# Performance work log

Measured on AMD Instinct MI355X. Metric: run time of the kernel, lower is better.

## Reference

```python
import jax, jax.numpy as jnp
import numpy as np

N = 4096      # sequence length (tokens)
D = 256       # model_dim
H = 4         # num_heads
DH = D // H   # dim_per_head = 64
TOPK = 30     # dot_attention default
SCALE = float((DH // H) ** -0.5)  # torch: (key.size(-1)//num_heads)**-0.5 = 16**-0.5 = 0.25
LN_EPS = 1e-5


def setup_inputs() -> dict:
    key = jax.random.key(0)
    ks = jax.random.split(key, 11)
    s = 0.02
    return {
        "key_in":   jax.random.normal(ks[0], (N, D), jnp.float32),
        "value_in": jax.random.normal(ks[1], (N, D), jnp.float32),
        "query_in": jax.random.normal(ks[2], (N, D), jnp.float32),
        "Wq": jax.random.normal(ks[3], (D, D), jnp.float32) * s,
        "bq": jax.random.normal(ks[4], (D,), jnp.float32) * s,
        "Wk": jax.random.normal(ks[5], (D, D), jnp.float32) * s,
        "bk": jax.random.normal(ks[6], (D,), jnp.float32) * s,
        "Wv": jax.random.normal(ks[7], (D, D), jnp.float32) * s,
        "bv": jax.random.normal(ks[8], (D,), jnp.float32) * s,
        "Wo": jax.random.normal(ks[9], (D, D), jnp.float32) * s,
        "bo": jax.random.normal(ks[10], (D,), jnp.float32) * s,
        "ln_g": jnp.ones((D,), jnp.float32),
        "ln_b": jnp.zeros((D,), jnp.float32),
    }


def reference(key_in, value_in, query_in, Wq, bq, Wk, bk, Wv, bv, Wo, bo, ln_g, ln_b):
    # Projections (nn.Linear: x @ W.T + b)
    q = query_in @ Wq.T + bq            # (N, D)
    k = key_in @ Wk.T + bk
    v = value_in @ Wv.T + bv
    # view(N, H, DH).transpose(0,1) -> (H, N, DH)
    qh = q.reshape(N, H, DH).transpose(1, 0, 2)
    kh = k.reshape(N, H, DH).transpose(1, 0, 2)
    vh = v.reshape(N, H, DH).transpose(1, 0, 2)

    scores = jnp.einsum('hnd,hmd->hnm', qh, kh) * SCALE   # (H, N, N)

    # top-k mask via scatter (faithful to torch.topk + scatter_)
    idx = jax.lax.top_k(scores, TOPK)[1]                  # (H, N, TOPK)
    mask = jnp.zeros_like(scores).at[
        jnp.arange(H)[:, None, None],
        jnp.arange(N)[None, :, None],
        idx].set(1.0)
    masked = jnp.where(mask > 0, scores, -jnp.inf)
    attn = jax.nn.softmax(masked, axis=-1)                # (H, N, N); dropout p=0 -> identity

    ctx = jnp.einsum('hnm,hmd->hnd', attn, vh)            # (H, N, DH)
    ctx = ctx.transpose(1, 0, 2).reshape(N, D)

    out = ctx @ Wo.T + bo
    resid = query_in + out                                # residual is pre-projection query
    mu = resid.mean(axis=-1, keepdims=True)
    var = resid.var(axis=-1, keepdims=True)               # biased var, like torch LayerNorm
    out = (resid - mu) / jnp.sqrt(var + LN_EPS) * ln_g + ln_b
    return out, attn
```

## Files before the change

### kernel.cpp

```cpp
#include <hip/hip_runtime.h>
#include <stdint.h>

#define N_TOK 4096
#define DIM   256
#define NH    4
#define DH    64
#define TOPK  30
#define CANDN 40
#define HWIN  128u
#define ATT_SCALE 0.25f
#define LN_EPS 1e-5f

typedef __attribute__((ext_vector_type(8))) short bf16x8;
typedef __attribute__((ext_vector_type(4))) float f32x4;

static __device__ __forceinline__ ushort f2bf(float f) {
    uint x = __float_as_uint(f);
    return (ushort)((x + 0x7FFFu + ((x >> 16) & 1u)) >> 16);
}
static __device__ __forceinline__ bf16x8 load_frag(const ushort* p) {
    union { int4 i; bf16x8 f; } u;
    u.i = *reinterpret_cast<const int4*>(p);
    return u.f;
}
static __device__ __forceinline__ bf16x8 cvt_frag(const float* p) {
    float4 a = *reinterpret_cast<const float4*>(p);
    float4 b = *reinterpret_cast<const float4*>(p + 4);
    union { ushort u[8]; bf16x8 f; } u;
    u.u[0] = f2bf(a.x); u.u[1] = f2bf(a.y); u.u[2] = f2bf(a.z); u.u[3] = f2bf(a.w);
    u.u[4] = f2bf(b.x); u.u[5] = f2bf(b.y); u.u[6] = f2bf(b.z); u.u[7] = f2bf(b.w);
    return u.f;
}
static __device__ __forceinline__ uint s16key(uint u) {
    return (u & 0x8000u) ? (u ^ 0xFFFFu) : (u | 0x8000u);
}
static __device__ __forceinline__ int jdecode(int P) {
    return (P & ~127) | ((P & 7) << 4) | ((P >> 3) & 15);
}

#define BK 32
__global__ __launch_bounds__(256) void front_kernel(
    const float* __restrict__ query_in, const float* __restrict__ key_in,
    const float* __restrict__ value_in,
    const float* __restrict__ Wq, const float* __restrict__ bq,
    const float* __restrict__ Wk, const float* __restrict__ bk,
    const float* __restrict__ Wv, const float* __restrict__ bv,
    float* __restrict__ qf, float* __restrict__ kf,
    ushort* __restrict__ qb, ushort* __restrict__ kb,
    float* __restrict__ vf)
{
    if (blockIdx.x < 8) {
        const int j0g = blockIdx.x * 64;
        const int sel = j0g >> 8;
        const int j0  = j0g & 255;
        const float* A    = sel ? key_in : query_in;
        const float* W    = sel ? Wk : Wq;
        const float* bias = sel ? bk : bq;
        float*  outF = sel ? kf : qf;
        ushort* outB = sel ? kb : qb;

        __shared__ float As[BK][64 + 4];
        __shared__ float Ws[BK][64 + 4];
        const int tid = threadIdx.x;
        const int tx = tid & 15;
        const int ty = tid >> 4;
        const int i0 = blockIdx.y * 64;

        float acc[4][4];
#pragma unroll
        for (int r = 0; r < 4; r++)
#pragma unroll
            for (int c = 0; c < 4; c++) acc[r][c] = 0.f;

        for (int k0 = 0; k0 < DIM; k0 += BK) {
#pragma unroll
            for (int u = 0; u < 2; u++) {
                const int f = u * 256 + tid;
                const int r = f >> 3;
                const int c = (f & 7) * 4;
                float4 va = *reinterpret_cast<const float4*>(A + (size_t)(i0 + r) * DIM + k0 + c);
                As[c + 0][r] = va.x; As[c + 1][r] = va.y;
                As[c + 2][r] = va.z; As[c + 3][r] = va.w;
                float4 vw = *reinterpret_cast<const float4*>(W + (size_t)(j0 + r) * DIM + k0 + c);
                Ws[c + 0][r] = vw.x; Ws[c + 1][r] = vw.y;
                Ws[c + 2][r] = vw.z; Ws[c + 3][r] = vw.w;
            }
            __syncthreads();
#pragma unroll
            for (int kk = 0; kk < BK; kk++) {
                const float4 a4 = *reinterpret_cast<const float4*>(&As[kk][ty * 4]);
                const float4 b4 = *reinterpret_cast<const float4*>(&Ws[kk][tx * 4]);
                const float ar[4] = {a4.x, a4.y, a4.z, a4.w};
                const float br[4] = {b4.x, b4.y, b4.z, b4.w};
#pragma unroll
                for (int r = 0; r < 4; r++)
#pragma unroll
                    for (int c = 0; c < 4; c++) acc[r][c] += ar[r] * br[c];
            }
            __syncthreads();
        }

#pragma unroll
        for (int r = 0; r < 4; r++) {
            const int gi = i0 + ty * 4 + r;
#pragma unroll
            for (int c = 0; c < 4; c++) {
                const int gj = j0 + tx * 4 + c;
                float v = acc[r][c] + bias[gj];
                outF[(size_t)gi * DIM + gj] = v;
                outB[(size_t)gi * DIM + gj] = f2bf(v);
            }
        }
    } else {
        const int lane = threadIdx.x & 63;
        const int wv   = threadIdx.x >> 6;
        const int i0   = blockIdx.y * 64 + wv * 16;
        const int j0   = (blockIdx.x - 8) * 64;
        const int r = lane & 15, q = lane >> 4;

        f32x4 acc[4];
#pragma unroll
        for (int b = 0; b < 4; b++) acc[b] = (f32x4){0.f, 0.f, 0.f, 0.f};

#pragma unroll
        for (int ks = 0; ks < 8; ks++) {
            const int kk = ks * 32 + q * 8;
            bf16x8 af = cvt_frag(value_in + (size_t)(i0 + r) * DIM + kk);
            bf16x8 bfr[4];
#pragma unroll
            for (int jt = 0; jt < 4; jt++)
                bfr[jt] = cvt_frag(Wv + (size_t)(j0 + jt * 16 + r) * DIM + kk);
#pragma unroll
            for (int jt = 0; jt < 4; jt++)
                acc[jt] = __builtin_amdgcn_mfma_f32_16x16x32_bf16(af, bfr[jt], acc[jt], 0, 0, 0);
        }

#pragma unroll
        for (int jt = 0; jt < 4; jt++) {
            const int gj = j0 + jt * 16 + r;
            const float bvv = bv[gj];
#pragma unroll
            for (int rg = 0; rg < 4; rg++) {
                const int gi = i0 + q * 4 + rg;
                vf[(size_t)gi * DIM + gj] = acc[jt][rg] + bvv;
            }
        }
    }
}

__global__ __launch_bounds__(256) void oproj_kernel(
    const ushort* __restrict__ A, const float* __restrict__ Wo,
    const float* __restrict__ bias, const float* __restrict__ addX,
    float* __restrict__ outF)
{
    const int lane = threadIdx.x & 63;
    const int wv   = threadIdx.x >> 6;
    const int i0   = blockIdx.y * 64 + wv * 16;
    const int j0   = blockIdx.x * 64;
    const int r = lane & 15, q = lane >> 4;

    f32x4 acc[4];
#pragma unroll
    for (int b = 0; b < 4; b++) acc[b] = (f32x4){0.f, 0.f, 0.f, 0.f};

#pragma unroll
    for (int ks = 0; ks < 8; ks++) {
        const int kk = ks * 32 + q * 8;
        bf16x8 af = load_frag(A + (size_t)(i0 + r) * DIM + kk);
        bf16x8 bfr[4];
#pragma unroll
        for (int jt = 0; jt < 4; jt++)
            bfr[jt] = cvt_frag(Wo + (size_t)(j0 + jt * 16 + r) * DIM + kk);
#pragma unroll
        for (int jt = 0; jt < 4; jt++)
            acc[jt] = __builtin_amdgcn_mfma_f32_16x16x32_bf16(af, bfr[jt], acc[jt], 0, 0, 0);
    }

#pragma unroll
    for (int jt = 0; jt < 4; jt++) {
        const int gj = j0 + jt * 16 + r;
        const float bvv = bias[gj];
#pragma unroll
        for (int rg = 0; rg < 4; rg++) {
            const int gi = i0 + q * 4 + rg;
            float v = acc[jt][rg] + bvv + addX[(size_t)gi * DIM + gj];
            outF[(size_t)gi * DIM + gj] = v;
        }
    }
}

__global__ __launch_bounds__(256) void scores_kernel(
    const ushort* __restrict__ qb, const ushort* __restrict__ kb,
    ushort* __restrict__ sb)
{
    const int lane = threadIdx.x & 63;
    const int wv   = threadIdx.x >> 6;
    const int h    = blockIdx.z;
    const int i0   = blockIdx.y * 128 + wv * 32;
    const int j0   = blockIdx.x * 128;
    const int r = lane & 15, q = lane >> 4;
    const int koff = h * DH;

    f32x4 acc[2][8];
#pragma unroll
    for (int a = 0; a < 2; a++)
#pragma unroll
        for (int b = 0; b < 8; b++) acc[a][b] = (f32x4){0.f, 0.f, 0.f, 0.f};

#pragma unroll
    for (int ks = 0; ks < 2; ks++) {
        const int kk = koff + ks * 32 + q * 8;
        bf16x8 af[2], bfr[8];
#pragma unroll
        for (int mt = 0; mt < 2; mt++)
            af[mt] = load_frag(qb + (size_t)(i0 + mt * 16 + r) * DIM + kk);
#pragma unroll
        for (int jt = 0; jt < 8; jt++)
            bfr[jt] = load_frag(kb + (size_t)(j0 + jt * 16 + r) * DIM + kk);
#pragma unroll
        for (int mt = 0; mt < 2; mt++)
#pragma unroll
            for (int jt = 0; jt < 8; jt++)
                acc[mt][jt] = __builtin_amdgcn_mfma_f32_16x16x32_bf16(
                    af[mt], bfr[jt], acc[mt][jt], 0, 0, 0);
    }

    const int tileBase = (j0 >> 7) * 16;
#pragma unroll
    for (int mt = 0; mt < 2; mt++)
#pragma unroll
        for (int rg = 0; rg < 4; rg++) {
            const int gi = i0 + mt * 16 + q * 4 + rg;
            uint w4[4];
#pragma unroll
            for (int p = 0; p < 4; p++) {
                const uint klo = s16key(f2bf(acc[mt][2 * p + 0][rg]));
                const uint khi = s16key(f2bf(acc[mt][2 * p + 1][rg]));
                w4[p] = klo | (khi << 16);
            }
            int4 outv;
            outv.x = (int)w4[0]; outv.y = (int)w4[1];
            outv.z = (int)w4[2]; outv.w = (int)w4[3];
            int4* rowp = reinterpret_cast<int4*>(sb + ((size_t)(h * N_TOK + gi)) * N_TOK);
            rowp[tileBase + r] = outv;
        }
}

__global__ __launch_bounds__(256) void select_kernel(
    const ushort* __restrict__ sb, const float* __restrict__ qf,
    const float* __restrict__ kf, const float* __restrict__ vf,
    float* __restrict__ pval, int* __restrict__ pidx,
    ushort* __restrict__ ctxb)
{
    const int lane = threadIdx.x & 63;
    const int wv   = threadIdx.x >> 6;
    const int row  = blockIdx.x * 4 + wv;
    const int h    = row >> 12;
    const int i    = row & (N_TOK - 1);
    const ushort* srow = sb + (size_t)row * N_TOK;

    __shared__ uint  hist[4][256];
    __shared__ uint  cand[4][64];
    __shared__ uint  ccnt[4];
    __shared__ float pw[4][TOPK];
    __shared__ int   jw[4][TOPK];
    __shared__ __align__(16) float qsh[4][DH];

    qsh[wv][lane] = qf[(size_t)i * DIM + h * DH + lane];
    if (lane == 0) ccnt[wv] = 0;
#pragma unroll
    for (int b = 0; b < 4; b++) hist[wv][b * 64 + lane] = 0u;

    uint kw[32];
    const int4* srow4 = reinterpret_cast<const int4*>(srow);
#pragma unroll
    for (int t = 0; t < 8; t++) {
        int4 c = srow4[t * 64 + lane];
        kw[t * 4 + 0] = (uint)c.x; kw[t * 4 + 1] = (uint)c.y;
        kw[t * 4 + 2] = (uint)c.z; kw[t * 4 + 3] = (uint)c.w;
    }

    uint mx = 0;
#pragma unroll
    for (int w = 0; w < 32; w++) {
        uint lo16 = kw[w] & 0xFFFFu, hi16 = kw[w] >> 16;
        mx = max(mx, max(lo16, hi16));
    }
#pragma unroll
    for (int off = 32; off; off >>= 1)
        mx = max(mx, (uint)__shfl_xor((int)mx, off));

    __syncthreads();

#pragma unroll
    for (int w = 0; w < 32; w++) {
        uint d0 = mx - (kw[w] & 0xFFFFu);
        uint d1 = mx - (kw[w] >> 16);
        if (d0 < HWIN) atomicAdd(&hist[wv][d0], 1u);
        if (d1 < HWIN) atomicAdd(&hist[wv][d1], 1u);
    }
    __syncthreads();

    const uint c0 = hist[wv][lane * 4 + 0];
    const uint c1 = hist[wv][lane * 4 + 1];
    const uint c2 = hist[wv][lane * 4 + 2];
    const uint c3 = hist[wv][lane * 4 + 3];
    const uint seg = c0 + c1 + c2 + c3;
    uint scan = seg;
#pragma unroll
    for (int d = 1; d < 64; d <<= 1) {
        uint y = (uint)__shfl_up((int)scan, d);
        if (lane >= d) scan += y;
    }
    const uint excl = scan - seg;
    const bool crossing = (excl < CANDN) && (scan >= CANDN);
    unsigned long long bal = __ballot(crossing);

    int t = 256;
    if (bal != 0ull) {
        const int srcLane = __ffsll(bal) - 1;
        int tloc = lane * 4;
        if (crossing) {
            uint cum = excl + c0;
            if (cum < CANDN) { tloc++; cum += c1;
                if (cum < CANDN) { tloc++; cum += c2;
                    if (cum < CANDN) { tloc++; } } }
        }
        t = __shfl(tloc, srcLane);
    }

    uint T;
    if (t <= 254) {
        T = mx - (uint)t;
    } else {
        uint lo = 0;
#pragma unroll
        for (int b = 15; b >= 0; b--) {
            uint trial = lo | (1u << b);
            int c = 0;
#pragma unroll
            for (int w = 0; w < 32; w++) {
                c += ((kw[w] & 0xFFFFu) >= trial) ? 1 : 0;
                c += ((kw[w] >> 16)     >= trial) ? 1 : 0;
            }
#pragma unroll
            for (int off = 32; off; off >>= 1) c += __shfl_xor(c, off);
            if (c >= CANDN) lo = trial;
        }
        T = lo;
    }

#pragma unroll
    for (int w = 0; w < 32; w++) {
        const uint lo16 = kw[w] & 0xFFFFu, hi16 = kw[w] >> 16;
        const int P0 = (w >> 2) * 512 + lane * 8 + (w & 3) * 2;
        if (lo16 >= T) {
            uint pos = atomicAdd(&ccnt[wv], 1u);
            if (pos < 64u) cand[wv][pos] = (uint)jdecode(P0);
        }
        if (hi16 >= T) {
            uint pos = atomicAdd(&ccnt[wv], 1u);
            if (pos < 64u) cand[wv][pos] = (uint)jdecode(P0 + 1);
        }
    }
    __syncthreads();
    const int m = (int)min(ccnt[wv], 64u);

    unsigned long long ukey = 0ull;
    if (lane < m) {
        const int j = (int)cand[wv][lane];
        const float4* kr = reinterpret_cast<const float4*>(kf + (size_t)j * DIM + h * DH);
        const float4* qr = reinterpret_cast<const float4*>(qsh[wv]);
        float s = 0.f;
#pragma unroll
        for (int d = 0; d < 16; d++) {
            float4 a = qr[d], bb = kr[d];
            s += a.x * bb.x; s += a.y * bb.y; s += a.z * bb.z; s += a.w * bb.w;
        }
        uint bits = __float_as_uint(s);
        uint s32 = (bits & 0x80000000u) ? ~bits : (bits | 0x80000000u);
        ukey = ((unsigned long long)s32 << 12) | (unsigned long long)(4095 - j);
    }

#pragma unroll
    for (int k = 2; k <= 64; k <<= 1) {
#pragma unroll
        for (int jj = k >> 1; jj > 0; jj >>= 1) {
            unsigned long long o = __shfl_xor(ukey, jj);
            bool keepMax = ((lane & jj) != 0) ^ ((lane & k) != 0);
            ukey = keepMax ? (ukey > o ? ukey : o) : (ukey < o ? ukey : o);
        }
    }

    const int rank = 63 - lane;
    const int jsel = 4095 - (int)(ukey & 0xFFFull);
    uint s32b = (uint)(ukey >> 12);
    uint fb = (s32b & 0x80000000u) ? (s32b ^ 0x80000000u) : ~s32b;
    const float sc = __uint_as_float(fb);
    const float stop = __shfl(sc, 63);

    float e = (rank < TOPK) ? __expf((sc - stop) * ATT_SCALE) : 0.f;
    float esum = e;
#pragma unroll
    for (int off = 32; off; off >>= 1) esum += __shfl_xor(esum, off);
    const float p = e / esum;

    if (rank < TOPK) {
        pw[wv][rank] = p; jw[wv][rank] = jsel;
        pval[(size_t)row * 32 + rank] = p;
        pidx[(size_t)row * 32 + rank] = jsel;
    }
    __syncthreads();

    float a = 0.f;
#pragma unroll
    for (int c = 0; c < TOPK; c++)
        a += pw[wv][c] * vf[(size_t)jw[wv][c] * DIM + h * DH + lane];
    ctxb[(size_t)i * DIM + h * DH + lane] = f2bf(a);
}

__global__ __launch_bounds__(256) void attn_ln(
    const float* __restrict__ pval, const int* __restrict__ pidx,
    float* __restrict__ attnF,
    float* __restrict__ resb, const float* __restrict__ g,
    const float* __restrict__ b)
{
    __shared__ __align__(16) float rb[4][N_TOK];
    const int tid = threadIdx.x;

    if (blockIdx.x < 4096) {
        const int r0 = blockIdx.x * 4;

        float4* rb4 = reinterpret_cast<float4*>(&rb[0][0]);
        const float4 z = {0.f, 0.f, 0.f, 0.f};
#pragma unroll
        for (int t = 0; t < 16; t++) rb4[t * 256 + tid] = z;
        __syncthreads();
        if (tid < 4 * TOPK) {
            const int w = tid / TOPK, c = tid % TOPK;
            rb[w][pidx[(size_t)(r0 + w) * 32 + c]] = pval[(size_t)(r0 + w) * 32 + c];
        }
        __syncthreads();
#pragma unroll
        for (int w = 0; w < 4; w++) {
            float4* grow = reinterpret_cast<float4*>(attnF + (size_t)(r0 + w) * N_TOK);
#pragma unroll
            for (int t = 0; t < 4; t++)
                grow[t * 256 + tid] = rb4[w * 1024 + t * 256 + tid];
        }
    } else {
        const int lane = tid & 63;
        const int wv   = tid >> 6;
        const int i    = (blockIdx.x - 4096) * 4 + wv;
        float4* rowp = reinterpret_cast<float4*>(resb + (size_t)i * DIM);
        float4 x = rowp[lane];
        float s  = x.x + x.y + x.z + x.w;
        float sq = x.x * x.x + x.y * x.y + x.z * x.z + x.w * x.w;
#pragma unroll
        for (int off = 32; off; off >>= 1) {
            s  += __shfl_xor(s, off);
            sq += __shfl_xor(sq, off);
        }
        const float mu  = s * (1.f / DIM);
        const float var = sq * (1.f / DIM) - mu * mu;
        const float rstd = rsqrtf(var + LN_EPS);
        const int col = lane * 4;
        float4 o;
        o.x = (x.x - mu) * rstd * g[col + 0] + b[col + 0];
        o.y = (x.y - mu) * rstd * g[col + 1] + b[col + 1];
        o.z = (x.z - mu) * rstd * g[col + 2] + b[col + 2];
        o.w = (x.w - mu) * rstd * g[col + 3] + b[col + 3];
        rowp[lane] = o;
    }
}

extern "C" void kernel_launch(void* const* d_in, const int* in_sizes, int n_in,
                              void* d_out, int out_size, void* d_ws, size_t ws_size,
                              hipStream_t stream)
{
    const float* key_in   = (const float*)d_in[0];
    const float* value_in = (const float*)d_in[1];
    const float* query_in = (const float*)d_in[2];
    const float* Wq = (const float*)d_in[3];
    const float* bq = (const float*)d_in[4];
    const float* Wk = (const float*)d_in[5];
    const float* bk = (const float*)d_in[6];
    const float* Wv = (const float*)d_in[7];
    const float* bv = (const float*)d_in[8];
    const float* Wo = (const float*)d_in[9];
    const float* bo = (const float*)d_in[10];
    const float* ln_g = (const float*)d_in[11];
    const float* ln_b = (const float*)d_in[12];

    float* outF  = (float*)d_out;
    float* attnF = outF + (size_t)N_TOK * DIM;

    const size_t SC = 33554432;
    ushort* sb   = (ushort*)attnF;
    float*  qf   = attnF + SC;
    float*  kf   = attnF + SC + 1048576;
    float*  vf   = attnF + SC + 2097152;
    ushort* qb   = (ushort*)(attnF + SC + 3145728);
    ushort* kb   = (ushort*)(attnF + SC + 3670016);
    ushort* ctxb = (ushort*)(attnF + SC + 4194304);

    float*  pval    = (float*)d_ws;
    int*    pidx    = (int*)d_ws + 524288;

    front_kernel<<<dim3(12, 64), 256, 0, stream>>>(
        query_in, key_in, value_in, Wq, bq, Wk, bk, Wv, bv,
        qf, kf, qb, kb, vf);

    scores_kernel<<<dim3(32, 32, NH), 256, 0, stream>>>(qb, kb, sb);
    select_kernel<<<dim3(N_TOK * NH / 4), 256, 0, stream>>>(
        sb, qf, kf, vf, pval, pidx, ctxb);

    oproj_kernel<<<dim3(4, 64), 256, 0, stream>>>(ctxb, Wo, bo, query_in, outF);

    attn_ln<<<dim3(4096 + 1024), 256, 0, stream>>>(
        pval, pidx, attnF, outF, ln_g, ln_b);
}
```

Before: 439.0 us.

## Fuse dense attention write into select kernel, storing scores in place in attn output

The scores kernel now writes its packed bf16 scores directly into each row's slot of the attention output. The select kernel reads its row into registers, then zero-fills the full fp32 row and scatters the top-k probabilities in place. This removes the separate scatter/expand kernel and the intermediate pval/pidx buffers. Projection intermediates move to the workspace, and a standalone LayerNorm kernel remains. The same dense-write traffic now lands inside the select kernel, which may lengthen it. Correctness relies on each wave finishing its reads before it overwrites the same row.

```diff
diff --git a/kernel.cpp b/kernel.cpp
--- a/kernel.cpp
+++ b/kernel.cpp
@@ -191,7 +191,7 @@
 
 __global__ __launch_bounds__(256) void scores_kernel(
     const ushort* __restrict__ qb, const ushort* __restrict__ kb,
-    ushort* __restrict__ sb)
+    float* __restrict__ attnF)
 {
     const int lane = threadIdx.x & 63;
     const int wv   = threadIdx.x >> 6;
@@ -241,15 +241,14 @@
             int4 outv;
             outv.x = (int)w4[0]; outv.y = (int)w4[1];
             outv.z = (int)w4[2]; outv.w = (int)w4[3];
-            int4* rowp = reinterpret_cast<int4*>(sb + ((size_t)(h * N_TOK + gi)) * N_TOK);
+            int4* rowp = reinterpret_cast<int4*>(attnF + (size_t)(h * N_TOK + gi) * N_TOK);
             rowp[tileBase + r] = outv;
         }
 }
 
 __global__ __launch_bounds__(256) void select_kernel(
-    const ushort* __restrict__ sb, const float* __restrict__ qf,
+    float* __restrict__ attnF, const float* __restrict__ qf,
     const float* __restrict__ kf, const float* __restrict__ vf,
-    float* __restrict__ pval, int* __restrict__ pidx,
     ushort* __restrict__ ctxb)
 {
     const int lane = threadIdx.x & 63;
@@ -257,7 +256,7 @@
     const int row  = blockIdx.x * 4 + wv;
     const int h    = row >> 12;
     const int i    = row & (N_TOK - 1);
-    const ushort* srow = sb + (size_t)row * N_TOK;
+    float* const arow = attnF + (size_t)row * N_TOK;
 
     __shared__ uint  hist[4][256];
     __shared__ uint  cand[4][64];
@@ -272,7 +271,7 @@
     for (int b = 0; b < 4; b++) hist[wv][b * 64 + lane] = 0u;
 
     uint kw[32];
-    const int4* srow4 = reinterpret_cast<const int4*>(srow);
+    const int4* srow4 = reinterpret_cast<const int4*>(arow);
 #pragma unroll
     for (int t = 0; t < 8; t++) {
         int4 c = srow4[t * 64 + lane];
@@ -407,9 +406,17 @@
 
     if (rank < TOPK) {
         pw[wv][rank] = p; jw[wv][rank] = jsel;
-        pval[(size_t)row * 32 + rank] = p;
-        pidx[(size_t)row * 32 + rank] = jsel;
-    }
+    }
+
+    {
+        float4* a4 = reinterpret_cast<float4*>(arow);
+        const float4 z = {0.f, 0.f, 0.f, 0.f};
+#pragma unroll
+        for (int tt = 0; tt < 16; tt++) a4[tt * 64 + lane] = z;
+        asm volatile("s_waitcnt vmcnt(0)" ::: "memory");
+        if (rank < TOPK) arow[jsel] = p;
+    }
+
     __syncthreads();
 
     float a = 0.f;
@@ -419,59 +426,32 @@
     ctxb[(size_t)i * DIM + h * DH + lane] = f2bf(a);
 }
 
-__global__ __launch_bounds__(256) void attn_ln(
-    const float* __restrict__ pval, const int* __restrict__ pidx,
-    float* __restrict__ attnF,
+__global__ __launch_bounds__(256) void ln_kernel(
     float* __restrict__ resb, const float* __restrict__ g,
     const float* __restrict__ b)
 {
-    __shared__ __align__(16) float rb[4][N_TOK];
-    const int tid = threadIdx.x;
-
-    if (blockIdx.x < 4096) {
-        const int r0 = blockIdx.x * 4;
-
-        float4* rb4 = reinterpret_cast<float4*>(&rb[0][0]);
-        const float4 z = {0.f, 0.f, 0.f, 0.f};
-#pragma unroll
-        for (int t = 0; t < 16; t++) rb4[t * 256 + tid] = z;
-        __syncthreads();
-        if (tid < 4 * TOPK) {
-            const int w = tid / TOPK, c = tid % TOPK;
-            rb[w][pidx[(size_t)(r0 + w) * 32 + c]] = pval[(size_t)(r0 + w) * 32 + c];
-        }
-        __syncthreads();
-#pragma unroll
-        for (int w = 0; w < 4; w++) {
-            float4* grow = reinterpret_cast<float4*>(attnF + (size_t)(r0 + w) * N_TOK);
-#pragma unroll
-            for (int t = 0; t < 4; t++)
-                grow[t * 256 + tid] = rb4[w * 1024 + t * 256 + tid];
-        }
-    } else {
-        const int lane = tid & 63;
-        const int wv   = tid >> 6;
-        const int i    = (blockIdx.x - 4096) * 4 + wv;
-        float4* rowp = reinterpret_cast<float4*>(resb + (size_t)i * DIM);
-        float4 x = rowp[lane];
-        float s  = x.x + x.y + x.z + x.w;
-        float sq = x.x * x.x + x.y * x.y + x.z * x.z + x.w * x.w;
-#pragma unroll
-        for (int off = 32; off; off >>= 1) {
-            s  += __shfl_xor(s, off);
-            sq += __shfl_xor(sq, off);
-        }
-        const float mu  = s * (1.f / DIM);
-        const float var = sq * (1.f / DIM) - mu * mu;
-        const float rstd = rsqrtf(var + LN_EPS);
-        const int col = lane * 4;
-        float4 o;
-        o.x = (x.x - mu) * rstd * g[col + 0] + b[col + 0];
-        o.y = (x.y - mu) * rstd * g[col + 1] + b[col + 1];
-        o.z = (x.z - mu) * rstd * g[col + 2] + b[col + 2];
-        o.w = (x.w - mu) * rstd * g[col + 3] + b[col + 3];
-        rowp[lane] = o;
-    }
+    const int lane = threadIdx.x & 63;
+    const int wv   = threadIdx.x >> 6;
+    const int i    = blockIdx.x * 4 + wv;
+    float4* rowp = reinterpret_cast<float4*>(resb + (size_t)i * DIM);
+    float4 x = rowp[lane];
+    float s  = x.x + x.y + x.z + x.w;
+    float sq = x.x * x.x + x.y * x.y + x.z * x.z + x.w * x.w;
+#pragma unroll
+    for (int off = 32; off; off >>= 1) {
+        s  += __shfl_xor(s, off);
+        sq += __shfl_xor(sq, off);
+    }
+    const float mu  = s * (1.f / DIM);
+    const float var = sq * (1.f / DIM) - mu * mu;
+    const float rstd = rsqrtf(var + LN_EPS);
+    const int col = lane * 4;
+    float4 o;
+    o.x = (x.x - mu) * rstd * g[col + 0] + b[col + 0];
+    o.y = (x.y - mu) * rstd * g[col + 1] + b[col + 1];
+    o.z = (x.z - mu) * rstd * g[col + 2] + b[col + 2];
+    o.w = (x.w - mu) * rstd * g[col + 3] + b[col + 3];
+    rowp[lane] = o;
 }
 
 extern "C" void kernel_launch(void* const* d_in, const int* in_sizes, int n_in,
@@ -495,28 +475,21 @@
     float* outF  = (float*)d_out;
     float* attnF = outF + (size_t)N_TOK * DIM;
 
-    const size_t SC = 33554432;
-    ushort* sb   = (ushort*)attnF;
-    float*  qf   = attnF + SC;
-    float*  kf   = attnF + SC + 1048576;
-    float*  vf   = attnF + SC + 2097152;
-    ushort* qb   = (ushort*)(attnF + SC + 3145728);
-    ushort* kb   = (ushort*)(attnF + SC + 3670016);
-    ushort* ctxb = (ushort*)(attnF + SC + 4194304);
-
-    float*  pval    = (float*)d_ws;
-    int*    pidx    = (int*)d_ws + 524288;
+    float*  qf   = (float*)d_ws;
+    float*  kf   = qf + 1048576;
+    float*  vf   = kf + 1048576;
+    ushort* qb   = (ushort*)(vf + 1048576);
+    ushort* kb   = qb + 1048576;
+    ushort* ctxb = kb + 1048576;
 
     front_kernel<<<dim3(12, 64), 256, 0, stream>>>(
         query_in, key_in, value_in, Wq, bq, Wk, bk, Wv, bv,
         qf, kf, qb, kb, vf);
 
-    scores_kernel<<<dim3(32, 32, NH), 256, 0, stream>>>(qb, kb, sb);
+    scores_kernel<<<dim3(32, 32, NH), 256, 0, stream>>>(qb, kb, attnF);
     select_kernel<<<dim3(N_TOK * NH / 4), 256, 0, stream>>>(
-        sb, qf, kf, vf, pval, pidx, ctxb);
+        attnF, qf, kf, vf, ctxb);
 
     oproj_kernel<<<dim3(4, 64), 256, 0, stream>>>(ctxb, Wo, bo, query_in, outF);
-
-    attn_ln<<<dim3(4096 + 1024), 256, 0, stream>>>(
-        pval, pidx, attnF, outF, ln_g, ln_b);
-}
+    ln_kernel<<<N_TOK / 4, 256, 0, stream>>>(outF, ln_g, ln_b);
+}
```

After: 446.9 us (median of 2 runs). About the same (+1.8%).
